# Performance work log

Measured on AMD Instinct MI355X. Metric: run time of the kernel, lower is better.

## Reference

```python
import jax, jax.numpy as jnp
import numpy as np

N = 50000      # nodes
E = 1600000    # directed edges (before self-loops)
H = 4          # heads for conv2/conv3


def feast(x, src, dst, W, u, c, b, heads, out_ch):
    """PyG FeaStConv: q = softmax((x_j - x_i) @ u + c) over heads,
    msg = sum_h q_h * (x_j @ W_h), mean-aggregated over in-neighbors, + bias.
    src/dst already include self-loops."""
    xj = x[src]                                   # [E', in]
    xi = x[dst]                                   # [E', in]
    q = jax.nn.softmax((xj - xi) @ u + c, axis=1)            # [E', H]
    t = (xj @ W).reshape(-1, heads, out_ch)                  # [E', H, out]
    m = jnp.einsum('ehc,eh->ec', t, q)                       # [E', out]
    s = jax.ops.segment_sum(m, dst, num_segments=N)          # [N, out]
    deg = jax.ops.segment_sum(jnp.ones((src.shape[0],), x.dtype), dst, num_segments=N)
    return s / jnp.maximum(deg, 1.0)[:, None] + b


def _glorot(k, shape):
    fan_in, fan_out = shape[0], shape[1] if len(shape) > 1 else shape[0]
    lim = np.sqrt(6.0 / (fan_in + fan_out))
    return jax.random.uniform(k, shape, jnp.float32, -lim, lim)


def setup_inputs() -> dict:
    key = jax.random.key(0)
    ks = jax.random.split(key, 32)
    d = {}
    d['x'] = jax.random.normal(ks[0], (N, 16), jnp.float32)
    d['edge_index'] = jax.random.randint(ks[1], (2, E), 0, N, jnp.int32)
    # conv2: 16->16, H=4 ; conv3: 16->16, H=4
    d['W2'] = _glorot(ks[2], (16, H * 16)); d['u2'] = _glorot(ks[3], (16, H))
    d['c2'] = jnp.zeros((H,), jnp.float32); d['b2'] = jnp.zeros((16,), jnp.float32)
    d['W3'] = _glorot(ks[4], (16, H * 16)); d['u3'] = _glorot(ks[5], (16, H))
    d['c3'] = jnp.zeros((H,), jnp.float32); d['b3'] = jnp.zeros((16,), jnp.float32)
    # conv4: 16->16 H=1 ; conv5: 16->32 H=1 ; conv6: 32->64 H=1
    d['W4'] = _glorot(ks[6], (16, 16)); d['u4'] = _glorot(ks[7], (16, 1))
    d['c4'] = jnp.zeros((1,), jnp.float32); d['b4'] = jnp.zeros((16,), jnp.float32)
    d['W5'] = _glorot(ks[8], (16, 32)); d['u5'] = _glorot(ks[9], (16, 1))
    d['c5'] = jnp.zeros((1,), jnp.float32); d['b5'] = jnp.zeros((32,), jnp.float32)
    d['W6'] = _glorot(ks[10], (32, 64)); d['u6'] = _glorot(ks[11], (32, 1))
    d['c6'] = jnp.zeros((1,), jnp.float32); d['b6'] = jnp.zeros((64,), jnp.float32)
    # MLP head: 64->16->4->1
    d['lw1'] = _glorot(ks[12], (64, 16)); d['lb1'] = jnp.zeros((16,), jnp.float32)
    d['lw2'] = _glorot(ks[13], (16, 4));  d['lb2'] = jnp.zeros((4,), jnp.float32)
    d['lw3'] = _glorot(ks[14], (4, 1));   d['lb3'] = jnp.zeros((1,), jnp.float32)
    return d


def reference(x, edge_index, W2, u2, c2, b2, W3, u3, c3, b3, W4, u4, c4, b4,
               W5, u5, c5, b5, W6, u6, c6, b6, lw1, lb1, lw2, lb2, lw3, lb3):
    loop = jnp.arange(N, dtype=edge_index.dtype)
    src = jnp.concatenate([edge_index[0], loop])   # self-loops (PyG default)
    dst = jnp.concatenate([edge_index[1], loop])
    h = jax.nn.relu(x)
    h = jax.nn.relu(feast(h, src, dst, W2, u2, c2, b2, H, 16))
    h = jax.nn.relu(feast(h, src, dst, W3, u3, c3, b3, H, 16))
    h = jax.nn.relu(feast(h, src, dst, W4, u4, c4, b4, 1, 16))
    h = jax.nn.relu(feast(h, src, dst, W5, u5, c5, b5, 1, 32))
    h = jax.nn.relu(feast(h, src, dst, W6, u6, c6, b6, 1, 64))
    h = jax.nn.relu(h @ lw1 + lb1)   # dropout disabled (eval mode)
    h = jax.nn.relu(h @ lw2 + lb2)
    return jax.nn.sigmoid(h @ lw3 + lb3)
```

## Files before the change

### kernel.cpp

```cpp
#include <hip/hip_runtime.h>
#include <hip/hip_fp16.h>
#include <math.h>


#define CAP 96
#define NPB 256
#define BCAP 10240

struct alignas(8)  H4 { __half2 lo, hi; };
struct alignas(16) H8 { __half2 a, b, c, d; };

__global__ void part_count(const int* __restrict__ dst, int E,
                           int* __restrict__ counts, int NB) {
    __shared__ int hist[256];
    for (int i = threadIdx.x; i < 256; i += blockDim.x) hist[i] = 0;
    __syncthreads();
    int nth = gridDim.x * blockDim.x;
    int tid = blockIdx.x * blockDim.x + threadIdx.x;
    int E4 = E >> 2;
    const int4* dst4 = (const int4*)dst;
    for (int e4 = tid; e4 < E4; e4 += nth) {
        int4 d = dst4[e4];
        atomicAdd(&hist[d.x >> 8], 1);
        atomicAdd(&hist[d.y >> 8], 1);
        atomicAdd(&hist[d.z >> 8], 1);
        atomicAdd(&hist[d.w >> 8], 1);
    }
    for (int e = (E4 << 2) + tid; e < E; e += nth)
        atomicAdd(&hist[dst[e] >> 8], 1);
    __syncthreads();
    for (int b = threadIdx.x; b < NB; b += blockDim.x)
        counts[b * NPB + blockIdx.x] = hist[b];
}

__global__ void part_scan(int* __restrict__ counts, int* __restrict__ bucketCnt) {
    __shared__ int s[NPB];
    int b = blockIdx.x;
    int t = threadIdx.x;
    int v = counts[b * NPB + t];
    s[t] = v;
    __syncthreads();
    for (int off = 1; off < NPB; off <<= 1) {
        int x = (t >= off) ? s[t - off] : 0;
        __syncthreads();
        s[t] += x;
        __syncthreads();
    }
    counts[b * NPB + t] = s[t] - v;
    if (t == NPB - 1) bucketCnt[b] = s[t];
}

__global__ void part_scatter(const int* __restrict__ src, const int* __restrict__ dst,
                             int E, const int* __restrict__ counts,
                             unsigned int* __restrict__ barr, int NB) {
    __shared__ int cur[256];
    for (int b = threadIdx.x; b < NB; b += blockDim.x)
        cur[b] = counts[b * NPB + blockIdx.x];
    __syncthreads();
    int nth = gridDim.x * blockDim.x;
    int tid = blockIdx.x * blockDim.x + threadIdx.x;
    int E4 = E >> 2;
    const int4* dst4 = (const int4*)dst;
    const int4* src4 = (const int4*)src;
    for (int e4 = tid; e4 < E4; e4 += nth) {
        int4 d = dst4[e4];
        int4 s = src4[e4];
        int p0 = atomicAdd(&cur[d.x >> 8], 1);
        barr[(size_t)(d.x >> 8) * BCAP + p0] = ((unsigned)(d.x & 255) << 16) | (unsigned)s.x;
        int p1 = atomicAdd(&cur[d.y >> 8], 1);
        barr[(size_t)(d.y >> 8) * BCAP + p1] = ((unsigned)(d.y & 255) << 16) | (unsigned)s.y;
        int p2 = atomicAdd(&cur[d.z >> 8], 1);
        barr[(size_t)(d.z >> 8) * BCAP + p2] = ((unsigned)(d.z & 255) << 16) | (unsigned)s.z;
        int p3 = atomicAdd(&cur[d.w >> 8], 1);
        barr[(size_t)(d.w >> 8) * BCAP + p3] = ((unsigned)(d.w & 255) << 16) | (unsigned)s.w;
    }
    for (int e = (E4 << 2) + tid; e < E; e += nth) {
        int d = dst[e];
        int pos = atomicAdd(&cur[d >> 8], 1);
        barr[(size_t)(d >> 8) * BCAP + pos] = ((unsigned)(d & 255) << 16) | (unsigned)src[e];
    }
}

__global__ void build_rows(const unsigned int* __restrict__ barr,
                           const int* __restrict__ bucketCnt,
                           int* __restrict__ padded, int* __restrict__ cnt, int N) {
    __shared__ int c[256];
    int b = blockIdx.x;
    int lo = b << 8;
    int nNodes = min(256, N - lo);
    for (int i = threadIdx.x; i < nNodes; i += blockDim.x) c[i] = 0;
    __syncthreads();
    int tot = bucketCnt[b];
    const unsigned int* be = barr + (size_t)b * BCAP;
    for (int e = threadIdx.x; e < tot; e += blockDim.x) {
        unsigned int pk = be[e];
        int dl = (int)(pk >> 16);
        int s  = (int)(pk & 0xFFFFu);
        int slot = atomicAdd(&c[dl], 1);
        padded[(size_t)(lo + dl) * CAP + slot] = s;
    }
    __syncthreads();
    for (int i = threadIdx.x; i < nNodes; i += blockDim.x) cnt[lo + i] = c[i];
}

template <bool RELU_IN>
__global__ void prep_h4(const float* __restrict__ h, const float* __restrict__ W,
                        const float* __restrict__ u, const float* __restrict__ cvec,
                        H4* __restrict__ TtH, float4* __restrict__ a4,
                        float4* __restrict__ b4, int N) {
    int t = blockIdx.x * blockDim.x + threadIdx.x;
    int i = t >> 4, c = t & 15;
    if (i >= N) return;
    const float4* hp = (const float4*)(h + (size_t)i * 16);
    float4 q0 = hp[0], q1 = hp[1], q2 = hp[2], q3 = hp[3];
    float hv[16] = {q0.x, q0.y, q0.z, q0.w, q1.x, q1.y, q1.z, q1.w,
                    q2.x, q2.y, q2.z, q2.w, q3.x, q3.y, q3.z, q3.w};
    if (RELU_IN) {
        #pragma unroll
        for (int k = 0; k < 16; ++k) hv[k] = fmaxf(hv[k], 0.f);
    }
    float4 tv = {0.f, 0.f, 0.f, 0.f};
    #pragma unroll
    for (int k = 0; k < 16; ++k) {
        const float* Wk = W + k * 64 + c;
        tv.x = fmaf(hv[k], Wk[0],  tv.x);
        tv.y = fmaf(hv[k], Wk[16], tv.y);
        tv.z = fmaf(hv[k], Wk[32], tv.z);
        tv.w = fmaf(hv[k], Wk[48], tv.w);
    }
    H4 o;
    o.lo = __floats2half2_rn(tv.x, tv.y);
    o.hi = __floats2half2_rn(tv.z, tv.w);
    TtH[(size_t)i * 16 + c] = o;
    float p0 = 0.f, p1 = 0.f, p2 = 0.f, p3 = 0.f;
    #pragma unroll
    for (int k = 0; k < 16; ++k) {
        const float* uk = u + k * 4;
        p0 = fmaf(hv[k], uk[0], p0);
        p1 = fmaf(hv[k], uk[1], p1);
        p2 = fmaf(hv[k], uk[2], p2);
        p3 = fmaf(hv[k], uk[3], p3);
    }
    if (c == 0) {
        float z0 = p0 + cvec[0], z1 = p1 + cvec[1];
        float z2 = p2 + cvec[2], z3 = p3 + cvec[3];
        float A = fmaxf(fmaxf(z0, z1), fmaxf(z2, z3));
        float4 av = {__expf(z0 - A), __expf(z1 - A), __expf(z2 - A), __expf(z3 - A)};
        a4[i] = av;
        float B = fminf(fminf(p0, p1), fminf(p2, p3));
        float4 bv = {__expf(B - p0), __expf(B - p1), __expf(B - p2), __expf(B - p3)};
        b4[i] = bv;
    }
}

__global__ void row_h4(const int* __restrict__ cnt, const int* __restrict__ padded,
                       const float4* __restrict__ a4, const float4* __restrict__ b4,
                       const H8* __restrict__ TtH8, const float* __restrict__ bvec,
                       float* __restrict__ out, int N) {
    int wid = (blockIdx.x * blockDim.x + threadIdx.x) >> 6;
    int lane = threadIdx.x & 63;
    if (wid >= N) return;
    const int i = wid;
    const int g = lane >> 3, c8 = lane & 7;
    const int nE = cnt[i];
    const int base = i * CAP;
    const float4 bv = b4[i];
    float acc0 = 0.f, acc1 = 0.f;
    #pragma unroll 4
    for (int e = g; e < nE; e += 8) {
        int s = padded[base + e];
        float4 av = a4[s];
        H8 v = TtH8[(size_t)s * 8 + c8];
        float2 f0 = __half22float2(v.a);
        float2 f1 = __half22float2(v.b);
        float2 f2 = __half22float2(v.c);
        float2 f3 = __half22float2(v.d);
        float w0 = av.x * bv.x, w1 = av.y * bv.y;
        float w2 = av.z * bv.z, w3 = av.w * bv.w;
        float inv = __builtin_amdgcn_rcpf((w0 + w1) + (w2 + w3));
        acc0 = fmaf(fmaf(w0, f0.x, fmaf(w1, f0.y, fmaf(w2, f1.x, w3 * f1.y))), inv, acc0);
        acc1 = fmaf(fmaf(w0, f2.x, fmaf(w1, f2.y, fmaf(w2, f3.x, w3 * f3.y))), inv, acc1);
    }
    acc0 += __shfl_xor(acc0, 8);  acc1 += __shfl_xor(acc1, 8);
    acc0 += __shfl_xor(acc0, 16); acc1 += __shfl_xor(acc1, 16);
    acc0 += __shfl_xor(acc0, 32); acc1 += __shfl_xor(acc1, 32);
    if (lane < 8) {
        float4 av = a4[i];
        H8 v = TtH8[(size_t)i * 8 + c8];
        float2 f0 = __half22float2(v.a);
        float2 f1 = __half22float2(v.b);
        float2 f2 = __half22float2(v.c);
        float2 f3 = __half22float2(v.d);
        float w0 = av.x * bv.x, w1 = av.y * bv.y;
        float w2 = av.z * bv.z, w3 = av.w * bv.w;
        float inv = __builtin_amdgcn_rcpf((w0 + w1) + (w2 + w3));
        float s0 = fmaf(w0, f0.x, fmaf(w1, f0.y, fmaf(w2, f1.x, w3 * f1.y))) * inv;
        float s1 = fmaf(w0, f2.x, fmaf(w1, f2.y, fmaf(w2, f3.x, w3 * f3.y))) * inv;
        float invd = 1.0f / (float)(nE + 1);
        out[(size_t)i * 16 + 2 * c8]     = fmaxf((acc0 + s0) * invd + bvec[2 * c8], 0.f);
        out[(size_t)i * 16 + 2 * c8 + 1] = fmaxf((acc1 + s1) * invd + bvec[2 * c8 + 1], 0.f);
    }
}

template <int IN, int OUT>
__global__ void row_lin(const int* __restrict__ cnt, const int* __restrict__ padded,
                        const float* __restrict__ h, const float* __restrict__ Wm,
                        const float* __restrict__ bvec, float* __restrict__ out, int N) {
    constexpr int LPE = IN / 8;
    constexpr int GRPS = 64 / LPE;
    int wid = (blockIdx.x * blockDim.x + threadIdx.x) >> 6;
    int lane = threadIdx.x & 63;
    if (wid >= N) return;
    const int i = wid;
    const int sub = lane & (LPE - 1);
    const int g = lane / LPE;
    const int nE = cnt[i];
    const int base = i * CAP;
    const float4* h4 = (const float4*)h;
    float acc[8] = {0.f, 0.f, 0.f, 0.f, 0.f, 0.f, 0.f, 0.f};
    #pragma unroll 2
    for (int e = g; e < nE; e += GRPS) {
        int s = padded[base + e];
        float4 v0 = h4[(size_t)s * (IN / 4) + sub * 2];
        float4 v1 = h4[(size_t)s * (IN / 4) + sub * 2 + 1];
        acc[0] += v0.x; acc[1] += v0.y; acc[2] += v0.z; acc[3] += v0.w;
        acc[4] += v1.x; acc[5] += v1.y; acc[6] += v1.z; acc[7] += v1.w;
    }
    if (g == 0) {
        float4 v0 = h4[(size_t)i * (IN / 4) + sub * 2];
        float4 v1 = h4[(size_t)i * (IN / 4) + sub * 2 + 1];
        acc[0] += v0.x; acc[1] += v0.y; acc[2] += v0.z; acc[3] += v0.w;
        acc[4] += v1.x; acc[5] += v1.y; acc[6] += v1.z; acc[7] += v1.w;
    }
    #pragma unroll
    for (int mask = LPE; mask < 64; mask <<= 1) {
        #pragma unroll
        for (int k = 0; k < 8; ++k) acc[k] += __shfl_xor(acc[k], mask);
    }
    float invd = 1.0f / (float)(nE + 1);
    float m[8];
    #pragma unroll
    for (int k = 0; k < 8; ++k) m[k] = acc[k] * invd;
    int o = (lane < OUT) ? lane : 0;
    float oacc = bvec[o];
    #pragma unroll
    for (int q = 0; q < LPE; ++q) {
        #pragma unroll
        for (int k = 0; k < 8; ++k)
            oacc = fmaf(__shfl(m[k], q), Wm[(8 * q + k) * OUT + o], oacc);
    }
    if (lane < OUT) out[(size_t)i * OUT + lane] = fmaxf(oacc, 0.f);
}

__global__ void mlp_kernel(const float* __restrict__ h,
                           const float* __restrict__ lw1, const float* __restrict__ lb1,
                           const float* __restrict__ lw2, const float* __restrict__ lb2,
                           const float* __restrict__ lw3, const float* __restrict__ lb3,
                           float* __restrict__ out, int N) {
    int i = blockIdx.x * blockDim.x + threadIdx.x;
    if (i >= N) return;
    float a1[16];
    #pragma unroll
    for (int o = 0; o < 16; ++o) a1[o] = lb1[o];
    const float4* h4 = (const float4*)(h + (size_t)i * 64);
    #pragma unroll 4
    for (int k4 = 0; k4 < 16; ++k4) {
        float4 v = h4[k4];
        int k = k4 * 4;
        #pragma unroll
        for (int o = 0; o < 16; ++o) {
            a1[o] += v.x * lw1[(k + 0) * 16 + o];
            a1[o] += v.y * lw1[(k + 1) * 16 + o];
            a1[o] += v.z * lw1[(k + 2) * 16 + o];
            a1[o] += v.w * lw1[(k + 3) * 16 + o];
        }
    }
    float a2[4];
    #pragma unroll
    for (int j = 0; j < 4; ++j) a2[j] = lb2[j];
    #pragma unroll
    for (int o = 0; o < 16; ++o) {
        float v = fmaxf(a1[o], 0.f);
        #pragma unroll
        for (int j = 0; j < 4; ++j) a2[j] += v * lw2[o * 4 + j];
    }
    float z = lb3[0];
    #pragma unroll
    for (int j = 0; j < 4; ++j) z += fmaxf(a2[j], 0.f) * lw3[j];
    out[i] = 1.0f / (1.0f + __expf(-z));
}

extern "C" void kernel_launch(void* const* d_in, const int* in_sizes, int n_in,
                              void* d_out, int out_size, void* d_ws, size_t ws_size,
                              hipStream_t stream) {
    const float* x  = (const float*)d_in[0];
    const int*   ei = (const int*)d_in[1];
    const int E = in_sizes[1] / 2;
    const int N = in_sizes[0] / 16;
    const int* src = ei;
    const int* dst = ei + E;

    const float* W2 = (const float*)d_in[2];
    const float* u2 = (const float*)d_in[3];
    const float* c2 = (const float*)d_in[4];
    const float* b2 = (const float*)d_in[5];
    const float* W3 = (const float*)d_in[6];
    const float* u3 = (const float*)d_in[7];
    const float* c3 = (const float*)d_in[8];
    const float* b3 = (const float*)d_in[9];
    const float* W4 = (const float*)d_in[10];
    const float* b4v = (const float*)d_in[13];
    const float* W5 = (const float*)d_in[14];
    const float* b5 = (const float*)d_in[17];
    const float* W6 = (const float*)d_in[18];
    const float* b6 = (const float*)d_in[21];
    const float* lw1 = (const float*)d_in[22];
    const float* lb1 = (const float*)d_in[23];
    const float* lw2 = (const float*)d_in[24];
    const float* lb2 = (const float*)d_in[25];
    const float* lw3 = (const float*)d_in[26];
    const float* lb3 = (const float*)d_in[27];

    const int NB = (N + 255) >> 8;

    float* bufA = (float*)d_ws;
    float* bufB = bufA + (size_t)N * 64;
    float4* a4  = (float4*)(bufB + (size_t)N * 64);
    float4* b4  = a4 + N;
    H4*    TtH  = (H4*)(b4 + N);
    int*   padded    = (int*)(TtH + (size_t)N * 16);
    int*   cnt       = padded + (size_t)N * CAP;
    unsigned int* barr = (unsigned int*)(cnt + N);
    int*   counts    = (int*)(barr + (size_t)NB * BCAP);
    int*   bucketCnt = counts + NB * NPB;

    const int BS = 256;
    const int rowBlocks = (N + 3) / 4;
    const int prepBlocks = (N * 16 + BS - 1) / BS;

    part_count<<<NPB, 1024, 0, stream>>>(dst, E, counts, NB);
    part_scan<<<NB, NPB, 0, stream>>>(counts, bucketCnt);
    part_scatter<<<NPB, 1024, 0, stream>>>(src, dst, E, counts, barr, NB);
    build_rows<<<NB, 512, 0, stream>>>(barr, bucketCnt, padded, cnt, N);

    prep_h4<true><<<prepBlocks, BS, 0, stream>>>(x, W2, u2, c2, TtH, a4, b4, N);
    row_h4<<<rowBlocks, BS, 0, stream>>>(cnt, padded, a4, b4, (const H8*)TtH, b2, bufB, N);

    prep_h4<false><<<prepBlocks, BS, 0, stream>>>(bufB, W3, u3, c3, TtH, a4, b4, N);
    row_h4<<<rowBlocks, BS, 0, stream>>>(cnt, padded, a4, b4, (const H8*)TtH, b3, bufA, N);

    row_lin<16, 16><<<rowBlocks, BS, 0, stream>>>(cnt, padded, bufA, W4, b4v, bufB, N);

    row_lin<16, 32><<<rowBlocks, BS, 0, stream>>>(cnt, padded, bufB, W5, b5, bufA, N);

    row_lin<32, 64><<<rowBlocks, BS, 0, stream>>>(cnt, padded, bufA, W6, b6, bufB, N);

    mlp_kernel<<<(N + BS - 1) / BS, BS, 0, stream>>>(bufB, lw1, lb1, lw2, lb2, lw3, lb3,
                                                     (float*)d_out, N);
}
```

Before: 268.1 us.

## Process two rows per wavefront and gather neighbor features in fp16

Row kernels now give each row half a wavefront, so one wave handles two destination rows, with fewer neighbor groups per row and deeper unrolling. The row_lin aggregations gather neighbor features from an fp16 copy of the activations, written by the previous layer alongside the fp32 output. The self-loop term still reads fp32. This targets gather bandwidth and idle lanes on low-degree rows, at the cost of fp16 rounding in the neighbor sums and extra half-precision stores.

After: 286.8 us. 7.0% more time.

```diff
diff --git a/kernel.cpp b/kernel.cpp
--- a/kernel.cpp
+++ b/kernel.cpp
@@ -153,21 +153,24 @@
     }
 }
 
-__global__ void row_h4(const int* __restrict__ cnt, const int* __restrict__ padded,
-                       const float4* __restrict__ a4, const float4* __restrict__ b4,
-                       const H8* __restrict__ TtH8, const float* __restrict__ bvec,
-                       float* __restrict__ out, int N) {
-    int wid = (blockIdx.x * blockDim.x + threadIdx.x) >> 6;
+__global__ __launch_bounds__(256, 4)
+void row_h4(const int* __restrict__ cnt, const int* __restrict__ padded,
+            const float4* __restrict__ a4, const float4* __restrict__ b4,
+            const H8* __restrict__ TtH8, const float* __restrict__ bvec,
+            float* __restrict__ out, __half* __restrict__ out16, int N) {
+    int pair = (blockIdx.x * blockDim.x + threadIdx.x) >> 6;
     int lane = threadIdx.x & 63;
-    if (wid >= N) return;
-    const int i = wid;
-    const int g = lane >> 3, c8 = lane & 7;
-    const int nE = cnt[i];
-    const int base = i * CAP;
+    int r = lane >> 5, sub = lane & 31;
+    int g = sub >> 3, c8 = sub & 7;
+    int row = pair * 2 + r;
+    bool ok = row < N;
+    int i = ok ? row : 0;
+    int nE = ok ? cnt[i] : 0;
+    int base = i * CAP;
     const float4 bv = b4[i];
     float acc0 = 0.f, acc1 = 0.f;
-    #pragma unroll 4
-    for (int e = g; e < nE; e += 8) {
+    #pragma unroll 8
+    for (int e = g; e < nE; e += 4) {
         int s = padded[base + e];
         float4 av = a4[s];
         H8 v = TtH8[(size_t)s * 8 + c8];
@@ -183,8 +186,7 @@
     }
     acc0 += __shfl_xor(acc0, 8);  acc1 += __shfl_xor(acc1, 8);
     acc0 += __shfl_xor(acc0, 16); acc1 += __shfl_xor(acc1, 16);
-    acc0 += __shfl_xor(acc0, 32); acc1 += __shfl_xor(acc1, 32);
-    if (lane < 8) {
+    if (ok && sub < 8) {
         float4 av = a4[i];
         H8 v = TtH8[(size_t)i * 8 + c8];
         float2 f0 = __half22float2(v.a);
@@ -197,43 +199,58 @@
         float s0 = fmaf(w0, f0.x, fmaf(w1, f0.y, fmaf(w2, f1.x, w3 * f1.y))) * inv;
         float s1 = fmaf(w0, f2.x, fmaf(w1, f2.y, fmaf(w2, f3.x, w3 * f3.y))) * inv;
         float invd = 1.0f / (float)(nE + 1);
-        out[(size_t)i * 16 + 2 * c8]     = fmaxf((acc0 + s0) * invd + bvec[2 * c8], 0.f);
-        out[(size_t)i * 16 + 2 * c8 + 1] = fmaxf((acc1 + s1) * invd + bvec[2 * c8 + 1], 0.f);
+        float r0 = fmaxf((acc0 + s0) * invd + bvec[2 * c8], 0.f);
+        float r1 = fmaxf((acc1 + s1) * invd + bvec[2 * c8 + 1], 0.f);
+        out[(size_t)i * 16 + 2 * c8]     = r0;
+        out[(size_t)i * 16 + 2 * c8 + 1] = r1;
+        if (out16) {
+            out16[(size_t)i * 16 + 2 * c8]     = __float2half(r0);
+            out16[(size_t)i * 16 + 2 * c8 + 1] = __float2half(r1);
+        }
     }
 }
 
 template <int IN, int OUT>
-__global__ void row_lin(const int* __restrict__ cnt, const int* __restrict__ padded,
-                        const float* __restrict__ h, const float* __restrict__ Wm,
-                        const float* __restrict__ bvec, float* __restrict__ out, int N) {
+__global__ __launch_bounds__(256, 4)
+void row_lin(const int* __restrict__ cnt, const int* __restrict__ padded,
+             const float* __restrict__ h32, const __half* __restrict__ h16,
+             const float* __restrict__ Wm, const float* __restrict__ bvec,
+             float* __restrict__ out, __half* __restrict__ out16, int N) {
     constexpr int LPE = IN / 8;
-    constexpr int GRPS = 64 / LPE;
-    int wid = (blockIdx.x * blockDim.x + threadIdx.x) >> 6;
+    constexpr int GR  = 32 / LPE;
+    int pair = (blockIdx.x * blockDim.x + threadIdx.x) >> 6;
     int lane = threadIdx.x & 63;
-    if (wid >= N) return;
-    const int i = wid;
-    const int sub = lane & (LPE - 1);
-    const int g = lane / LPE;
-    const int nE = cnt[i];
-    const int base = i * CAP;
-    const float4* h4 = (const float4*)h;
+    int r = lane >> 5, sub = lane & 31;
+    int pe = sub & (LPE - 1);
+    int g = sub / LPE;
+    int row = pair * 2 + r;
+    bool ok = row < N;
+    int i = ok ? row : 0;
+    int nE = ok ? cnt[i] : 0;
+    int base = i * CAP;
+    const H8* hp = (const H8*)h16;
     float acc[8] = {0.f, 0.f, 0.f, 0.f, 0.f, 0.f, 0.f, 0.f};
-    #pragma unroll 2
-    for (int e = g; e < nE; e += GRPS) {
+    #pragma unroll 4
+    for (int e = g; e < nE; e += GR) {
         int s = padded[base + e];
-        float4 v0 = h4[(size_t)s * (IN / 4) + sub * 2];
-        float4 v1 = h4[(size_t)s * (IN / 4) + sub * 2 + 1];
+        H8 v = hp[(size_t)s * LPE + pe];
+        float2 f0 = __half22float2(v.a);
+        float2 f1 = __half22float2(v.b);
+        float2 f2 = __half22float2(v.c);
+        float2 f3 = __half22float2(v.d);
+        acc[0] += f0.x; acc[1] += f0.y;
+        acc[2] += f1.x; acc[3] += f1.y;
+        acc[4] += f2.x; acc[5] += f2.y;
+        acc[6] += f3.x; acc[7] += f3.y;
+    }
+    if (ok && g == 0) {
+        const float4* s4 = (const float4*)(h32 + (size_t)i * IN);
+        float4 v0 = s4[pe * 2], v1 = s4[pe * 2 + 1];
         acc[0] += v0.x; acc[1] += v0.y; acc[2] += v0.z; acc[3] += v0.w;
         acc[4] += v1.x; acc[5] += v1.y; acc[6] += v1.z; acc[7] += v1.w;
     }
-    if (g == 0) {
-        float4 v0 = h4[(size_t)i * (IN / 4) + sub * 2];
-        float4 v1 = h4[(size_t)i * (IN / 4) + sub * 2 + 1];
-        acc[0] += v0.x; acc[1] += v0.y; acc[2] += v0.z; acc[3] += v0.w;
-        acc[4] += v1.x; acc[5] += v1.y; acc[6] += v1.z; acc[7] += v1.w;
-    }
-    #pragma unroll
-    for (int mask = LPE; mask < 64; mask <<= 1) {
+    #pragma unroll
+    for (int mask = LPE; mask < 32; mask <<= 1) {
         #pragma unroll
         for (int k = 0; k < 8; ++k) acc[k] += __shfl_xor(acc[k], mask);
     }
@@ -241,15 +258,37 @@
     float m[8];
     #pragma unroll
     for (int k = 0; k < 8; ++k) m[k] = acc[k] * invd;
-    int o = (lane < OUT) ? lane : 0;
-    float oacc = bvec[o];
-    #pragma unroll
-    for (int q = 0; q < LPE; ++q) {
-        #pragma unroll
-        for (int k = 0; k < 8; ++k)
-            oacc = fmaf(__shfl(m[k], q), Wm[(8 * q + k) * OUT + o], oacc);
-    }
-    if (lane < OUT) out[(size_t)i * OUT + lane] = fmaxf(oacc, 0.f);
+    if (OUT <= 32) {
+        int o = (sub < OUT) ? sub : 0;
+        float oacc = bvec[o];
+        #pragma unroll
+        for (int q = 0; q < LPE; ++q) {
+            #pragma unroll
+            for (int k = 0; k < 8; ++k)
+                oacc = fmaf(__shfl(m[k], r * 32 + q), Wm[(8 * q + k) * OUT + o], oacc);
+        }
+        if (ok && sub < OUT) {
+            float rr = fmaxf(oacc, 0.f);
+            out[(size_t)i * OUT + sub] = rr;
+            if (out16) out16[(size_t)i * OUT + sub] = __float2half(rr);
+        }
+    } else {
+        int o0 = sub, o1 = sub + 32;
+        float oa = bvec[o0], ob = bvec[o1];
+        #pragma unroll
+        for (int q = 0; q < LPE; ++q) {
+            #pragma unroll
+            for (int k = 0; k < 8; ++k) {
+                float mv = __shfl(m[k], r * 32 + q);
+                oa = fmaf(mv, Wm[(8 * q + k) * OUT + o0], oa);
+                ob = fmaf(mv, Wm[(8 * q + k) * OUT + o1], ob);
+            }
+        }
+        if (ok) {
+            out[(size_t)i * OUT + o0] = fmaxf(oa, 0.f);
+            out[(size_t)i * OUT + o1] = fmaxf(ob, 0.f);
+        }
+    }
 }
 
 __global__ void mlp_kernel(const float* __restrict__ h,
@@ -328,14 +367,16 @@
     float4* a4  = (float4*)(bufB + (size_t)N * 64);
     float4* b4  = a4 + N;
     H4*    TtH  = (H4*)(b4 + N);
-    int*   padded    = (int*)(TtH + (size_t)N * 16);
+    __half* bufAh = (__half*)(TtH + (size_t)N * 16);
+    __half* bufBh = bufAh + (size_t)N * 32;
+    int*   padded    = (int*)(bufBh + (size_t)N * 16);
     int*   cnt       = padded + (size_t)N * CAP;
     unsigned int* barr = (unsigned int*)(cnt + N);
     int*   counts    = (int*)(barr + (size_t)NB * BCAP);
     int*   bucketCnt = counts + NB * NPB;
 
     const int BS = 256;
-    const int rowBlocks = (N + 3) / 4;
+    const int pairBlocks = ((N + 1) / 2 + 3) / 4;
     const int prepBlocks = (N * 16 + BS - 1) / BS;
 
     part_count<<<NPB, 1024, 0, stream>>>(dst, E, counts, NB);
@@ -344,16 +385,21 @@
     build_rows<<<NB, 512, 0, stream>>>(barr, bucketCnt, padded, cnt, N);
 
     prep_h4<true><<<prepBlocks, BS, 0, stream>>>(x, W2, u2, c2, TtH, a4, b4, N);
-    row_h4<<<rowBlocks, BS, 0, stream>>>(cnt, padded, a4, b4, (const H8*)TtH, b2, bufB, N);
+    row_h4<<<pairBlocks, BS, 0, stream>>>(cnt, padded, a4, b4, (const H8*)TtH, b2,
+                                          bufB, nullptr, N);
 
     prep_h4<false><<<prepBlocks, BS, 0, stream>>>(bufB, W3, u3, c3, TtH, a4, b4, N);
-    row_h4<<<rowBlocks, BS, 0, stream>>>(cnt, padded, a4, b4, (const H8*)TtH, b3, bufA, N);
-
-    row_lin<16, 16><<<rowBlocks, BS, 0, stream>>>(cnt, padded, bufA, W4, b4v, bufB, N);
-
-    row_lin<16, 32><<<rowBlocks, BS, 0, stream>>>(cnt, padded, bufB, W5, b5, bufA, N);
-
-    row_lin<32, 64><<<rowBlocks, BS, 0, stream>>>(cnt, padded, bufA, W6, b6, bufB, N);
+    row_h4<<<pairBlocks, BS, 0, stream>>>(cnt, padded, a4, b4, (const H8*)TtH, b3,
+                                          bufA, bufAh, N);
+
+    row_lin<16, 16><<<pairBlocks, BS, 0, stream>>>(cnt, padded, bufA, bufAh, W4, b4v,
+                                                   bufB, bufBh, N);
+
+    row_lin<16, 32><<<pairBlocks, BS, 0, stream>>>(cnt, padded, bufB, bufBh, W5, b5,
+                                                   bufA, bufAh, N);
+
+    row_lin<32, 64><<<pairBlocks, BS, 0, stream>>>(cnt, padded, bufA, bufAh, W6, b6,
+                                                   bufB, nullptr, N);
 
     mlp_kernel<<<(N + BS - 1) / BS, BS, 0, stream>>>(bufB, lw1, lb1, lw2, lb2, lw3, lb3,
                                                      (float*)d_out, N);
```
